# Kernel tuning notes

Hardware: AMD Instinct MI355X
Metric: run time of the kernel (lower is better)

## Reference

```python
import jax, jax.numpy as jnp
import numpy as np

TOP_K = 2


def setup_inputs() -> dict:
    key = jax.random.key(0)
    k1, k2, k3, k4 = jax.random.split(key, 4)
    B, S, H, I, E = 2, 2048, 1024, 2048, 8
    x = jax.random.normal(k1, (B, S, H), dtype=jnp.float32)
    router_w = jax.random.normal(k2, (E, H), dtype=jnp.float32) * 0.02
    w1 = jax.random.normal(k3, (E, 2 * I, H), dtype=jnp.float32) * 0.01
    w2 = jax.random.normal(k4, (E, H, I), dtype=jnp.float32) * 0.01
    return {"x": x, "router_w": router_w, "w1": w1, "w2": w2}


def reference(x, router_w, w1, w2):
    B, S, H = x.shape
    E = w1.shape[0]
    I = w2.shape[2]
    xf = x.reshape(-1, H)                       # [T, H]
    T = xf.shape[0]

    # --- TopK router ---
    logits = xf @ router_w.T                    # [T, E]
    probs = jax.nn.softmax(logits, axis=-1)
    rw, sel = jax.lax.top_k(probs, TOP_K)       # [T, K]
    rw = rw.astype(jnp.float32)
    rw = rw / jnp.sum(rw, axis=-1, keepdims=True)

    # dense per-token expert combine weights [T, E] (zero for unselected experts)
    wmat = jnp.zeros((T, E), dtype=jnp.float32)
    wmat = wmat.at[jnp.arange(T)[:, None], sel].add(rw)

    # --- SwiGLU expert FFN + weighted combine (loop over small fixed E) ---
    out = jnp.zeros((T, H), dtype=x.dtype)
    for e in range(E):
        h = xf @ w1[e].T                        # [T, 2I]
        gate, up = h[:, :I], h[:, I:]
        act = jax.nn.silu(gate) * up            # [T, I]
        oe = act @ w2[e].T                      # [T, H]
        out = out + wmat[:, e:e + 1] * oe
    return out.reshape(B, S, H)
```

## Files before the change

kernel.cpp:

```cpp
#include <hip/hip_runtime.h>

#define TT 4096
#define HH 1024
#define EE 8
#define II 2048
#define NP 8192

typedef unsigned short u16;
typedef __attribute__((ext_vector_type(8))) short bf16x8;
typedef __attribute__((ext_vector_type(4))) float f32x4;

__device__ __forceinline__ u16 f2b(float f) {
  union { float f; unsigned u; } v; v.f = f;
  unsigned u = v.u;
  u += 0x7fffu + ((u >> 16) & 1u);
  return (u16)(u >> 16);
}
__device__ __forceinline__ float b2f(u16 b) {
  union { unsigned u; float f; } v; v.u = ((unsigned)b) << 16;
  return v.f;
}

typedef const __attribute__((address_space(1))) unsigned int ga_u32;
typedef __attribute__((address_space(3))) unsigned int lds_u32;
__device__ __forceinline__ void async16(const void* g, void* l) {
  __builtin_amdgcn_global_load_lds((ga_u32*)g, (lds_u32*)l, 16, 0, 0);
}

__global__ void cvt_kernel(const float* __restrict__ src, u16* __restrict__ dst, int n) {
  int i = (blockIdx.x * blockDim.x + threadIdx.x) * 4;
  int stride = gridDim.x * blockDim.x * 4;
  for (; i < n; i += stride) {
    float4 v = *(const float4*)(src + i);
    ushort4 o;
    o.x = f2b(v.x); o.y = f2b(v.y); o.z = f2b(v.z); o.w = f2b(v.w);
    *(ushort4*)(dst + i) = o;
  }
}

__global__ void router_kernel(const float* __restrict__ xf, const float* __restrict__ rw,
                              int* __restrict__ sel, float* __restrict__ selw,
                              int* __restrict__ cnt) {
  const int wid = threadIdx.x >> 6;
  const int lane = threadIdx.x & 63;
  const int t = blockIdx.x * 4 + wid;
  if (t >= TT) return;
  float acc[EE];
  #pragma unroll
  for (int e = 0; e < EE; e++) acc[e] = 0.f;
  const float* xp = xf + (size_t)t * HH;
  for (int k = lane; k < HH; k += 64) {
    float xv = xp[k];
    #pragma unroll
    for (int e = 0; e < EE; e++) acc[e] += xv * rw[e * HH + k];
  }
  #pragma unroll
  for (int e = 0; e < EE; e++) {
    float v = acc[e];
    #pragma unroll
    for (int off = 32; off > 0; off >>= 1) v += __shfl_xor(v, off, 64);
    acc[e] = v;
  }
  if (lane == 0) {
    float m = acc[0];
    #pragma unroll
    for (int e = 1; e < EE; e++) m = fmaxf(m, acc[e]);
    float p[EE];
    #pragma unroll
    for (int e = 0; e < EE; e++) p[e] = __expf(acc[e] - m);
    int e1 = 0;
    #pragma unroll
    for (int e = 1; e < EE; e++) if (p[e] > p[e1]) e1 = e;
    int e2 = -1;
    #pragma unroll
    for (int e = 0; e < EE; e++) {
      if (e == e1) continue;
      if (e2 < 0 || p[e] > p[e2]) e2 = e;
    }
    float s = p[e1] + p[e2];
    sel[t * 2] = e1; sel[t * 2 + 1] = e2;
    selw[t * 2] = p[e1] / s; selw[t * 2 + 1] = p[e2] / s;
    atomicAdd(&cnt[e1], 1);
    atomicAdd(&cnt[e2], 1);
  }
}

__global__ void prefix_kernel(const int* __restrict__ cnt, int* __restrict__ base) {
  int s = 0;
  for (int e = 0; e < EE; e++) { base[e] = s; s += cnt[e]; }
}

__global__ void scatter_kernel(const int* __restrict__ sel, const float* __restrict__ selw,
                               const int* __restrict__ base, int* __restrict__ fill,
                               int* __restrict__ ptok, float* __restrict__ pwt,
                               int* __restrict__ prow) {
  int t = blockIdx.x * blockDim.x + threadIdx.x;
  if (t >= TT) return;
  #pragma unroll
  for (int k = 0; k < 2; k++) {
    int e = sel[t * 2 + k];
    int slot = atomicAdd(&fill[e], 1);
    int row = base[e] + slot;
    ptok[row] = t;
    pwt[row] = selw[t * 2 + k];
    prow[t * 2 + k] = row;
  }
}

__global__ __launch_bounds__(256, 2)
void gemm1_kernel(const u16* __restrict__ xb, const u16* __restrict__ w1b,
                  const int* __restrict__ ptok, const int* __restrict__ cnt,
                  const int* __restrict__ base, u16* __restrict__ actb) {
  const int e = blockIdx.z, mt = blockIdx.y, nt = blockIdx.x;
  const int mc = cnt[e];
  if (mt * 128 >= mc) return;
  const int mb = base[e];
  __shared__ u16 lA[128 * 32];
  __shared__ u16 lBg[128 * 32];
  __shared__ u16 lBu[128 * 32];
  const int tid = threadIdx.x;
  const int lane = tid & 63;
  const int wid = tid >> 6;
  const int wm = wid >> 1, wn = wid & 1;
  const int r0 = tid >> 2, c0 = (tid & 3) * 8;
  int i0 = mb + mt * 128 + r0;
  int i1 = i0 + 64;
  i0 = min(i0, NP - 1); i1 = min(i1, NP - 1);
  const size_t t0 = (size_t)ptok[i0], t1 = (size_t)ptok[i1];
  const u16* a0 = xb + t0 * HH + c0;
  const u16* a1 = xb + t1 * HH + c0;
  const u16* bg0 = w1b + (size_t)e * (2 * II) * HH + (size_t)(nt * 128 + r0) * HH + c0;
  const u16* bg1 = bg0 + (size_t)64 * HH;
  const u16* bu0 = bg0 + (size_t)II * HH;
  const u16* bu1 = bu0 + (size_t)64 * HH;
  u16* la0 = &lA[r0 * 32 + c0];
  u16* la1 = &lA[(r0 + 64) * 32 + c0];
  u16* lg0 = &lBg[r0 * 32 + c0];
  u16* lg1 = &lBg[(r0 + 64) * 32 + c0];
  u16* lu0 = &lBu[r0 * 32 + c0];
  u16* lu1 = &lBu[(r0 + 64) * 32 + c0];
  f32x4 accg[4][4], accu[4][4];
  #pragma unroll
  for (int m = 0; m < 4; m++)
    #pragma unroll
    for (int n = 0; n < 4; n++) {
      accg[m][n] = f32x4{0.f, 0.f, 0.f, 0.f};
      accu[m][n] = f32x4{0.f, 0.f, 0.f, 0.f};
    }
  const int lr = lane & 15, lk = (lane >> 4) * 8;
  for (int kt = 0; kt < HH / 32; kt++) {
    async16(a0 + kt * 32, la0);
    async16(a1 + kt * 32, la1);
    async16(bg0 + kt * 32, lg0);
    async16(bg1 + kt * 32, lg1);
    async16(bu0 + kt * 32, lu0);
    async16(bu1 + kt * 32, lu1);
    __syncthreads();
    bf16x8 af[4], gf[4], uf[4];
    #pragma unroll
    for (int m = 0; m < 4; m++)
      af[m] = *(const bf16x8*)&lA[(wm * 64 + m * 16 + lr) * 32 + lk];
    #pragma unroll
    for (int n = 0; n < 4; n++) {
      gf[n] = *(const bf16x8*)&lBg[(wn * 64 + n * 16 + lr) * 32 + lk];
      uf[n] = *(const bf16x8*)&lBu[(wn * 64 + n * 16 + lr) * 32 + lk];
    }
    #pragma unroll
    for (int m = 0; m < 4; m++)
      #pragma unroll
      for (int n = 0; n < 4; n++) {
        accg[m][n] = __builtin_amdgcn_mfma_f32_16x16x32_bf16(af[m], gf[n], accg[m][n], 0, 0, 0);
        accu[m][n] = __builtin_amdgcn_mfma_f32_16x16x32_bf16(af[m], uf[n], accu[m][n], 0, 0, 0);
      }
    __syncthreads();
  }
  const int lrow = (lane >> 4) * 4;
  #pragma unroll
  for (int m = 0; m < 4; m++) {
    #pragma unroll
    for (int j = 0; j < 4; j++) {
      const int rl = wm * 64 + m * 16 + lrow + j;
      const int rg = mt * 128 + rl;
      if (rg < mc) {
        u16* op = actb + (size_t)(mb + rg) * II + nt * 128 + wn * 64 + lr;
        #pragma unroll
        for (int n = 0; n < 4; n++) {
          float g = accg[m][n][j], u = accu[m][n][j];
          op[n * 16] = f2b(u * g / (1.f + __expf(-g)));
        }
      }
    }
  }
}

__global__ __launch_bounds__(256, 2)
void gemm2_kernel(const u16* __restrict__ actb, const u16* __restrict__ w2b,
                  const int* __restrict__ cnt, const int* __restrict__ base,
                  u16* __restrict__ oe) {
  const int e = blockIdx.z, mt = blockIdx.y, nt = blockIdx.x;
  const int mc = cnt[e];
  if (mt * 128 >= mc) return;
  const int mb = base[e];
  __shared__ u16 lA[128 * 32];
  __shared__ u16 lB[128 * 32];
  const int tid = threadIdx.x;
  const int lane = tid & 63;
  const int wid = tid >> 6;
  const int wm = wid >> 1, wn = wid & 1;
  const int r0 = tid >> 2, c0 = (tid & 3) * 8;
  const u16* a0 = actb + (size_t)(mb + mt * 128 + r0) * II + c0;
  const u16* a1 = a0 + (size_t)64 * II;
  const u16* b0 = w2b + (size_t)e * HH * II + (size_t)(nt * 128 + r0) * II + c0;
  const u16* b1 = b0 + (size_t)64 * II;
  u16* la0 = &lA[r0 * 32 + c0];
  u16* la1 = &lA[(r0 + 64) * 32 + c0];
  u16* lb0 = &lB[r0 * 32 + c0];
  u16* lb1 = &lB[(r0 + 64) * 32 + c0];
  f32x4 acc[4][4];
  #pragma unroll
  for (int m = 0; m < 4; m++)
    #pragma unroll
    for (int n = 0; n < 4; n++) acc[m][n] = f32x4{0.f, 0.f, 0.f, 0.f};
  const int lr = lane & 15, lk = (lane >> 4) * 8;
  for (int kt = 0; kt < II / 32; kt++) {
    async16(a0 + kt * 32, la0);
    async16(a1 + kt * 32, la1);
    async16(b0 + kt * 32, lb0);
    async16(b1 + kt * 32, lb1);
    __syncthreads();
    bf16x8 af[4], bfr[4];
    #pragma unroll
    for (int m = 0; m < 4; m++)
      af[m] = *(const bf16x8*)&lA[(wm * 64 + m * 16 + lr) * 32 + lk];
    #pragma unroll
    for (int n = 0; n < 4; n++)
      bfr[n] = *(const bf16x8*)&lB[(wn * 64 + n * 16 + lr) * 32 + lk];
    #pragma unroll
    for (int m = 0; m < 4; m++)
      #pragma unroll
      for (int n = 0; n < 4; n++)
        acc[m][n] = __builtin_amdgcn_mfma_f32_16x16x32_bf16(af[m], bfr[n], acc[m][n], 0, 0, 0);
    __syncthreads();
  }
  const int lrow = (lane >> 4) * 4;
  #pragma unroll
  for (int m = 0; m < 4; m++) {
    #pragma unroll
    for (int j = 0; j < 4; j++) {
      const int rl = wm * 64 + m * 16 + lrow + j;
      const int rg = mt * 128 + rl;
      if (rg < mc) {
        u16* op = oe + (size_t)(mb + rg) * HH + nt * 128 + wn * 64 + lr;
        #pragma unroll
        for (int n = 0; n < 4; n++) op[n * 16] = f2b(acc[m][n][j]);
      }
    }
  }
}

__global__ void combine_kernel(const u16* __restrict__ oe, const int* __restrict__ prow,
                               const float* __restrict__ pwt, float* __restrict__ out) {
  int idx = blockIdx.x * blockDim.x + threadIdx.x;
  const int chunks = HH / 8;
  if (idx >= TT * chunks) return;
  int t = idx / chunks;
  int c = (idx % chunks) * 8;
  int ra = prow[t * 2], rb = prow[t * 2 + 1];
  float wa = pwt[ra], wb = pwt[rb];
  const ushort4* pa = (const ushort4*)(oe + (size_t)ra * HH + c);
  const ushort4* pb = (const ushort4*)(oe + (size_t)rb * HH + c);
  float4* po = (float4*)(out + (size_t)t * HH + c);
  #pragma unroll
  for (int h = 0; h < 2; h++) {
    ushort4 va = pa[h], vb = pb[h];
    float4 o;
    o.x = wa * b2f(va.x) + wb * b2f(vb.x);
    o.y = wa * b2f(va.y) + wb * b2f(vb.y);
    o.z = wa * b2f(va.z) + wb * b2f(vb.z);
    o.w = wa * b2f(va.w) + wb * b2f(vb.w);
    po[h] = o;
  }
}

extern "C" void kernel_launch(void* const* d_in, const int* in_sizes, int n_in,
                              void* d_out, int out_size, void* d_ws, size_t ws_size,
                              hipStream_t stream) {
  (void)in_sizes; (void)n_in; (void)out_size; (void)ws_size;
  const float* x  = (const float*)d_in[0];
  const float* rw = (const float*)d_in[1];
  const float* w1 = (const float*)d_in[2];
  const float* w2 = (const float*)d_in[3];
  float* out = (float*)d_out;
  char* ws = (char*)d_ws;
  size_t off = 0;
  u16* xb   = (u16*)(ws + off); off += (size_t)TT * HH * 2;
  u16* w1b  = (u16*)(ws + off); off += (size_t)EE * 2 * II * HH * 2;
  u16* w2b  = (u16*)(ws + off); off += (size_t)EE * HH * II * 2;
  u16* actb = (u16*)(ws + off); off += (size_t)NP * II * 2;
  u16* oe   = (u16*)(ws + off); off += (size_t)NP * HH * 2;
  int*   ptok = (int*)(ws + off);   off += (size_t)NP * 4;
  float* pwt  = (float*)(ws + off); off += (size_t)NP * 4;
  int*   prow = (int*)(ws + off);   off += (size_t)NP * 4;
  int*   sel  = (int*)(ws + off);   off += (size_t)TT * 2 * 4;
  float* selw = (float*)(ws + off); off += (size_t)TT * 2 * 4;
  int* cnt   = (int*)(ws + off); off += 32;
  int* fill  = (int*)(ws + off); off += 32;
  int* basep = (int*)(ws + off); off += 32;

  hipMemsetAsync(cnt, 0, 96, stream);

  cvt_kernel<<<2048, 256, 0, stream>>>(x,  xb,  TT * HH);
  cvt_kernel<<<4096, 256, 0, stream>>>(w1, w1b, EE * 2 * II * HH);
  cvt_kernel<<<4096, 256, 0, stream>>>(w2, w2b, EE * HH * II);

  router_kernel<<<TT / 4, 256, 0, stream>>>(x, rw, sel, selw, cnt);
  prefix_kernel<<<1, 1, 0, stream>>>(cnt, basep);
  scatter_kernel<<<TT / 256, 256, 0, stream>>>(sel, selw, basep, fill, ptok, pwt, prow);

  gemm1_kernel<<<dim3(16, 64, 8), 256, 0, stream>>>(xb, w1b, ptok, cnt, basep, actb);
  gemm2_kernel<<<dim3(8, 64, 8), 256, 0, stream>>>(actb, w2b, cnt, basep, oe);
  combine_kernel<<<(TT * (HH / 8) + 255) / 256, 256, 0, stream>>>(oe, prow, pwt, out);
}
```

Baseline: 611.6 us.

## Double-buffer GEMM LDS tiles and launch compact tile list for grouped experts

```diff
diff --git a/kernel.cpp b/kernel.cpp
--- a/kernel.cpp
+++ b/kernel.cpp
@@ -5,6 +5,7 @@
 #define EE 8
 #define II 2048
 #define NP 8192
+#define MAXTILES 72
 
 typedef unsigned short u16;
 typedef __attribute__((ext_vector_type(8))) short bf16x8;
@@ -39,8 +40,7 @@
 }
 
 __global__ void router_kernel(const float* __restrict__ xf, const float* __restrict__ rw,
-                              int* __restrict__ sel, float* __restrict__ selw,
-                              int* __restrict__ cnt) {
+                              int* __restrict__ sel, float* __restrict__ selw) {
   const int wid = threadIdx.x >> 6;
   const int lane = threadIdx.x & 63;
   const int t = blockIdx.x * 4 + wid;
@@ -80,44 +80,63 @@
     float s = p[e1] + p[e2];
     sel[t * 2] = e1; sel[t * 2 + 1] = e2;
     selw[t * 2] = p[e1] / s; selw[t * 2 + 1] = p[e2] / s;
-    atomicAdd(&cnt[e1], 1);
-    atomicAdd(&cnt[e2], 1);
-  }
-}
-
-__global__ void prefix_kernel(const int* __restrict__ cnt, int* __restrict__ base) {
-  int s = 0;
-  for (int e = 0; e < EE; e++) { base[e] = s; s += cnt[e]; }
+  }
+}
+
+__global__ void count_kernel(const int* __restrict__ sel, int* __restrict__ cnt) {
+  int idx = blockIdx.x * blockDim.x + threadIdx.x;
+  int e = (idx < NP) ? sel[idx] : -1;
+  #pragma unroll
+  for (int ee = 0; ee < EE; ee++) {
+    if (e == ee) atomicAdd(&cnt[ee], 1);
+  }
+}
+
+__global__ void prefix_kernel(const int* __restrict__ cnt, int* __restrict__ base,
+                              int* __restrict__ tile_e, int* __restrict__ tile_m,
+                              int* __restrict__ n_tiles) {
+  int s = 0, nt = 0;
+  for (int e = 0; e < EE; e++) {
+    base[e] = s;
+    int c = cnt[e];
+    for (int m = 0; m * 128 < c; m++) { tile_e[nt] = e; tile_m[nt] = m; nt++; }
+    s += c;
+  }
+  *n_tiles = nt;
 }
 
 __global__ void scatter_kernel(const int* __restrict__ sel, const float* __restrict__ selw,
                                const int* __restrict__ base, int* __restrict__ fill,
                                int* __restrict__ ptok, float* __restrict__ pwt,
                                int* __restrict__ prow) {
-  int t = blockIdx.x * blockDim.x + threadIdx.x;
-  if (t >= TT) return;
-  #pragma unroll
-  for (int k = 0; k < 2; k++) {
-    int e = sel[t * 2 + k];
-    int slot = atomicAdd(&fill[e], 1);
-    int row = base[e] + slot;
-    ptok[row] = t;
-    pwt[row] = selw[t * 2 + k];
-    prow[t * 2 + k] = row;
-  }
-}
-
+  int idx = blockIdx.x * blockDim.x + threadIdx.x;
+  if (idx >= NP) return;
+  int t = idx >> 1;
+  int e = sel[idx];
+  #pragma unroll
+  for (int ee = 0; ee < EE; ee++) {
+    if (e == ee) {
+      int slot = atomicAdd(&fill[ee], 1);
+      int row = base[ee] + slot;
+      ptok[row] = t;
+      pwt[row] = selw[idx];
+      prow[idx] = row;
+    }
+  }
+}
+
+#define G1SEG 4096
 __global__ __launch_bounds__(256, 2)
 void gemm1_kernel(const u16* __restrict__ xb, const u16* __restrict__ w1b,
                   const int* __restrict__ ptok, const int* __restrict__ cnt,
-                  const int* __restrict__ base, u16* __restrict__ actb) {
-  const int e = blockIdx.z, mt = blockIdx.y, nt = blockIdx.x;
-  const int mc = cnt[e];
-  if (mt * 128 >= mc) return;
-  const int mb = base[e];
-  __shared__ u16 lA[128 * 32];
-  __shared__ u16 lBg[128 * 32];
-  __shared__ u16 lBu[128 * 32];
+                  const int* __restrict__ base,
+                  const int* __restrict__ tile_e, const int* __restrict__ tile_m,
+                  const int* __restrict__ n_tiles, u16* __restrict__ actb) {
+  const int ti = blockIdx.y;
+  if (ti >= *n_tiles) return;
+  const int e = tile_e[ti], mt = tile_m[ti], nt = blockIdx.x;
+  const int mc = cnt[e], mb = base[e];
+  __shared__ u16 L[2][3 * G1SEG];
   const int tid = threadIdx.x;
   const int lane = tid & 63;
   const int wid = tid >> 6;
@@ -133,12 +152,8 @@
   const u16* bg1 = bg0 + (size_t)64 * HH;
   const u16* bu0 = bg0 + (size_t)II * HH;
   const u16* bu1 = bu0 + (size_t)64 * HH;
-  u16* la0 = &lA[r0 * 32 + c0];
-  u16* la1 = &lA[(r0 + 64) * 32 + c0];
-  u16* lg0 = &lBg[r0 * 32 + c0];
-  u16* lg1 = &lBg[(r0 + 64) * 32 + c0];
-  u16* lu0 = &lBu[r0 * 32 + c0];
-  u16* lu1 = &lBu[(r0 + 64) * 32 + c0];
+  const int o0 = r0 * 32 + c0;
+  const int o1 = (r0 + 64) * 32 + c0;
   f32x4 accg[4][4], accu[4][4];
   #pragma unroll
   for (int m = 0; m < 4; m++)
@@ -148,22 +163,30 @@
       accu[m][n] = f32x4{0.f, 0.f, 0.f, 0.f};
     }
   const int lr = lane & 15, lk = (lane >> 4) * 8;
-  for (int kt = 0; kt < HH / 32; kt++) {
-    async16(a0 + kt * 32, la0);
-    async16(a1 + kt * 32, la1);
-    async16(bg0 + kt * 32, lg0);
-    async16(bg1 + kt * 32, lg1);
-    async16(bu0 + kt * 32, lu0);
-    async16(bu1 + kt * 32, lu1);
-    __syncthreads();
+
+  #define G1STAGE(b, kt) { u16* Lb = &L[b][0];                 \
+    async16(a0  + (kt) * 32, Lb + o0);                          \
+    async16(a1  + (kt) * 32, Lb + o1);                          \
+    async16(bg0 + (kt) * 32, Lb + G1SEG + o0);                  \
+    async16(bg1 + (kt) * 32, Lb + G1SEG + o1);                  \
+    async16(bu0 + (kt) * 32, Lb + 2 * G1SEG + o0);              \
+    async16(bu1 + (kt) * 32, Lb + 2 * G1SEG + o1); }
+
+  G1STAGE(0, 0);
+  __syncthreads();
+  int cur = 0;
+  const int NT = HH / 32;
+  for (int kt = 0; kt < NT; ++kt) {
+    if (kt + 1 < NT) G1STAGE(cur ^ 1, kt + 1);
+    const u16* Lb = &L[cur][0];
     bf16x8 af[4], gf[4], uf[4];
     #pragma unroll
     for (int m = 0; m < 4; m++)
-      af[m] = *(const bf16x8*)&lA[(wm * 64 + m * 16 + lr) * 32 + lk];
+      af[m] = *(const bf16x8*)(Lb + (wm * 64 + m * 16 + lr) * 32 + lk);
     #pragma unroll
     for (int n = 0; n < 4; n++) {
-      gf[n] = *(const bf16x8*)&lBg[(wn * 64 + n * 16 + lr) * 32 + lk];
-      uf[n] = *(const bf16x8*)&lBu[(wn * 64 + n * 16 + lr) * 32 + lk];
+      gf[n] = *(const bf16x8*)(Lb + G1SEG + (wn * 64 + n * 16 + lr) * 32 + lk);
+      uf[n] = *(const bf16x8*)(Lb + 2 * G1SEG + (wn * 64 + n * 16 + lr) * 32 + lk);
     }
     #pragma unroll
     for (int m = 0; m < 4; m++)
@@ -173,6 +196,7 @@
         accu[m][n] = __builtin_amdgcn_mfma_f32_16x16x32_bf16(af[m], uf[n], accu[m][n], 0, 0, 0);
       }
     __syncthreads();
+    cur ^= 1;
   }
   const int lrow = (lane >> 4) * 4;
   #pragma unroll
@@ -193,16 +217,17 @@
   }
 }
 
+#define G2SEG 4096
 __global__ __launch_bounds__(256, 2)
 void gemm2_kernel(const u16* __restrict__ actb, const u16* __restrict__ w2b,
                   const int* __restrict__ cnt, const int* __restrict__ base,
-                  u16* __restrict__ oe) {
-  const int e = blockIdx.z, mt = blockIdx.y, nt = blockIdx.x;
-  const int mc = cnt[e];
-  if (mt * 128 >= mc) return;
-  const int mb = base[e];
-  __shared__ u16 lA[128 * 32];
-  __shared__ u16 lB[128 * 32];
+                  const int* __restrict__ tile_e, const int* __restrict__ tile_m,
+                  const int* __restrict__ n_tiles, u16* __restrict__ oe) {
+  const int ti = blockIdx.y;
+  if (ti >= *n_tiles) return;
+  const int e = tile_e[ti], mt = tile_m[ti], nt = blockIdx.x;
+  const int mc = cnt[e], mb = base[e];
+  __shared__ u16 L[2][2 * G2SEG];
   const int tid = threadIdx.x;
   const int lane = tid & 63;
   const int wid = tid >> 6;
@@ -212,35 +237,42 @@
   const u16* a1 = a0 + (size_t)64 * II;
   const u16* b0 = w2b + (size_t)e * HH * II + (size_t)(nt * 128 + r0) * II + c0;
   const u16* b1 = b0 + (size_t)64 * II;
-  u16* la0 = &lA[r0 * 32 + c0];
-  u16* la1 = &lA[(r0 + 64) * 32 + c0];
-  u16* lb0 = &lB[r0 * 32 + c0];
-  u16* lb1 = &lB[(r0 + 64) * 32 + c0];
+  const int o0 = r0 * 32 + c0;
+  const int o1 = (r0 + 64) * 32 + c0;
   f32x4 acc[4][4];
   #pragma unroll
   for (int m = 0; m < 4; m++)
     #pragma unroll
     for (int n = 0; n < 4; n++) acc[m][n] = f32x4{0.f, 0.f, 0.f, 0.f};
   const int lr = lane & 15, lk = (lane >> 4) * 8;
-  for (int kt = 0; kt < II / 32; kt++) {
-    async16(a0 + kt * 32, la0);
-    async16(a1 + kt * 32, la1);
-    async16(b0 + kt * 32, lb0);
-    async16(b1 + kt * 32, lb1);
-    __syncthreads();
+
+  #define G2STAGE(b, kt) { u16* Lb = &L[b][0];                 \
+    async16(a0 + (kt) * 32, Lb + o0);                           \
+    async16(a1 + (kt) * 32, Lb + o1);                           \
+    async16(b0 + (kt) * 32, Lb + G2SEG + o0);                   \
+    async16(b1 + (kt) * 32, Lb + G2SEG + o1); }
+
+  G2STAGE(0, 0);
+  __syncthreads();
+  int cur = 0;
+  const int NT = II / 32;
+  for (int kt = 0; kt < NT; ++kt) {
+    if (kt + 1 < NT) G2STAGE(cur ^ 1, kt + 1);
+    const u16* Lb = &L[cur][0];
     bf16x8 af[4], bfr[4];
     #pragma unroll
     for (int m = 0; m < 4; m++)
-      af[m] = *(const bf16x8*)&lA[(wm * 64 + m * 16 + lr) * 32 + lk];
+      af[m] = *(const bf16x8*)(Lb + (wm * 64 + m * 16 + lr) * 32 + lk);
     #pragma unroll
     for (int n = 0; n < 4; n++)
-      bfr[n] = *(const bf16x8*)&lB[(wn * 64 + n * 16 + lr) * 32 + lk];
+      bfr[n] = *(const bf16x8*)(Lb + G2SEG + (wn * 64 + n * 16 + lr) * 32 + lk);
     #pragma unroll
     for (int m = 0; m < 4; m++)
       #pragma unroll
       for (int n = 0; n < 4; n++)
         acc[m][n] = __builtin_amdgcn_mfma_f32_16x16x32_bf16(af[m], bfr[n], acc[m][n], 0, 0, 0);
     __syncthreads();
+    cur ^= 1;
   }
   const int lrow = (lane >> 4) * 4;
   #pragma unroll
@@ -296,28 +328,34 @@
   u16* xb   = (u16*)(ws + off); off += (size_t)TT * HH * 2;
   u16* w1b  = (u16*)(ws + off); off += (size_t)EE * 2 * II * HH * 2;
   u16* w2b  = (u16*)(ws + off); off += (size_t)EE * HH * II * 2;
-  u16* actb = (u16*)(ws + off); off += (size_t)NP * II * 2;
+  u16* actb = (u16*)(ws + off); off += (size_t)(NP + 128) * II * 2;
   u16* oe   = (u16*)(ws + off); off += (size_t)NP * HH * 2;
   int*   ptok = (int*)(ws + off);   off += (size_t)NP * 4;
   float* pwt  = (float*)(ws + off); off += (size_t)NP * 4;
   int*   prow = (int*)(ws + off);   off += (size_t)NP * 4;
   int*   sel  = (int*)(ws + off);   off += (size_t)TT * 2 * 4;
   float* selw = (float*)(ws + off); off += (size_t)TT * 2 * 4;
-  int* cnt   = (int*)(ws + off); off += 32;
-  int* fill  = (int*)(ws + off); off += 32;
-  int* basep = (int*)(ws + off); off += 32;
-
-  hipMemsetAsync(cnt, 0, 96, stream);
+  int* cnt    = (int*)(ws + off); off += 32 * 4;
+  int* fill   = (int*)(ws + off); off += 32 * 4;
+  int* basep  = (int*)(ws + off); off += 32 * 4;
+  int* tile_e = (int*)(ws + off); off += MAXTILES * 4;
+  int* tile_m = (int*)(ws + off); off += MAXTILES * 4;
+  int* ntile  = (int*)(ws + off); off += 16;
+
+  hipMemsetAsync(cnt, 0, 64 * 4, stream);
 
   cvt_kernel<<<2048, 256, 0, stream>>>(x,  xb,  TT * HH);
   cvt_kernel<<<4096, 256, 0, stream>>>(w1, w1b, EE * 2 * II * HH);
   cvt_kernel<<<4096, 256, 0, stream>>>(w2, w2b, EE * HH * II);
 
-  router_kernel<<<TT / 4, 256, 0, stream>>>(x, rw, sel, selw, cnt);
-  prefix_kernel<<<1, 1, 0, stream>>>(cnt, basep);
-  scatter_kernel<<<TT / 256, 256, 0, stream>>>(sel, selw, basep, fill, ptok, pwt, prow);
-
-  gemm1_kernel<<<dim3(16, 64, 8), 256, 0, stream>>>(xb, w1b, ptok, cnt, basep, actb);
-  gemm2_kernel<<<dim3(8, 64, 8), 256, 0, stream>>>(actb, w2b, cnt, basep, oe);
+  router_kernel<<<TT / 4, 256, 0, stream>>>(x, rw, sel, selw);
+  count_kernel<<<NP / 256, 256, 0, stream>>>(sel, cnt);
+  prefix_kernel<<<1, 1, 0, stream>>>(cnt, basep, tile_e, tile_m, ntile);
+  scatter_kernel<<<NP / 256, 256, 0, stream>>>(sel, selw, basep, fill, ptok, pwt, prow);
+
+  gemm1_kernel<<<dim3(16, MAXTILES), 256, 0, stream>>>(xb, w1b, ptok, cnt, basep,
+                                                       tile_e, tile_m, ntile, actb);
+  gemm2_kernel<<<dim3(8, MAXTILES), 256, 0, stream>>>(actb, w2b, cnt, basep,
+                                                      tile_e, tile_m, ntile, oe);
   combine_kernel<<<(TT * (HH / 8) + 255) / 256, 256, 0, stream>>>(oe, prow, pwt, out);
 }
```

Result: faster. 490.0 us (-19.9%).
